# Kernel optimization log

Hardware: AMD Instinct MI355X
Metric: run time of the kernel (lower is better)

The kernel has to match this reference:

```python
import jax, jax.numpy as jnp
import numpy as np

B, N, D, H = 4, 4096, 128, 8
DH = D // H
EPS = 1e-6


def _layernorm(x, g, b):
    mu = jnp.mean(x, axis=-1, keepdims=True)
    var = jnp.var(x, axis=-1, keepdims=True)
    return (x - mu) * jax.lax.rsqrt(var + EPS) * g + b


def setup_inputs() -> dict:
    key = jax.random.key(0)
    ks = jax.random.split(key, 12)
    p = lambda k, shape: (jax.random.normal(k, shape, jnp.float32) * 0.02)
    x = jax.random.normal(ks[0], (B, N, D), jnp.float32)
    # scale fx so the sigmoid of the N-length contraction is not fully saturated
    fx = jax.random.normal(ks[1], (B, N, D), jnp.float32) / N
    return {
        "x": x,
        "fx": fx,
        "ln1_g": jnp.ones((D,), jnp.float32),
        "ln1_b": jnp.zeros((D,), jnp.float32),
        "wq": p(ks[2], (D, D)),
        "wk": p(ks[3], (D, D)),
        "wv": p(ks[4], (D, D)),
        "wo": p(ks[5], (D, D)),
        "bo": jnp.zeros((D,), jnp.float32),
        "ln2_g": jnp.ones((D,), jnp.float32),
        "ln2_b": jnp.zeros((D,), jnp.float32),
        "w1": p(ks[6], (D, D)),
        "b1": jnp.zeros((D,), jnp.float32),
        "w2": p(ks[7], (D, D)),
        "b2": jnp.zeros((D,), jnp.float32),
    }


def reference(x, fx, ln1_g, ln1_b, wq, wk, wv, wo, bo, ln2_g, ln2_b, w1, b1, w2, b2):
    b, n, d = x.shape
    h, dh = H, d // H
    # --- pre-norm linear self-attention ---
    xn = _layernorm(x, ln1_g, ln1_b)
    def heads(w):  # [b,n,d] @ w^T -> [b,h,n,dh]
        return jnp.einsum('bnd,ed->bne', xn, w).reshape(b, n, h, dh).transpose(0, 2, 1, 3)
    q = jax.nn.softmax(heads(wq), axis=-1)   # softmax over feature dim
    k = jax.nn.softmax(heads(wk), axis=2)    # softmax over sequence dim
    v = heads(wv)
    ctx = jnp.einsum('bhnd,bhne->bhde', k, v)         # [b,h,dh,dh]
    attn = jnp.einsum('bhnd,bhde->bhne', q, ctx)       # [b,h,n,dh]
    attn = attn.transpose(0, 2, 1, 3).reshape(b, n, d)
    attn = jnp.einsum('bnd,ed->bne', attn, wo) + bo
    x = x + attn                                       # residual (dropout=identity)
    # --- pre-norm MLP ---
    y = _layernorm(x, ln2_g, ln2_b)
    y = jax.nn.gelu(jnp.einsum('bnd,ed->bne', y, w1) + b1, approximate=False)
    y = jnp.einsum('bnd,ed->bne', y, w2) + b2
    x = x + y
    # --- quadratic update: sigmoid((x x^T) fx), as written in the module ---
    gram = jnp.einsum('bnd,bmd->bnm', x, x)            # [b,n,n] materialized, faithful
    fx = jax.nn.sigmoid(jnp.einsum('bnm,bmd->bnd', gram, fx))
    return (x, fx)
```

## Files before the change

### kernel.cpp

```cpp
#include <hip/hip_runtime.h>
#include <math.h>

#define BB 4
#define NN 4096
#define DD 128
#define MM (BB*NN)

typedef __attribute__((ext_vector_type(8))) short short8;
typedef __attribute__((ext_vector_type(4))) float f32x4;

__device__ inline short f2bf(float f) {
    unsigned u = __float_as_uint(f);
    u = (u + 0x7FFFu + ((u >> 16) & 1u)) >> 16;
    return (short)u;
}
__device__ inline float bf2f(short s) {
    return __uint_as_float(((unsigned)(unsigned short)s) << 16);
}
__device__ inline short8 pack_bf8(float4 a, float4 b) {
    short8 o;
    o[0] = f2bf(a.x); o[1] = f2bf(a.y); o[2] = f2bf(a.z); o[3] = f2bf(a.w);
    o[4] = f2bf(b.x); o[5] = f2bf(b.y); o[6] = f2bf(b.z); o[7] = f2bf(b.w);
    return o;
}
__device__ inline int swzoff(int row, int col) {
    return ((row * 128 + col) * 2) ^ ((row & 7) << 4);
}

__global__ __launch_bounds__(256) void wprep(const float* __restrict__ w0, const float* __restrict__ w1,
                                             const float* __restrict__ w2, const float* __restrict__ w3,
                                             const float* __restrict__ w4, short* __restrict__ wf) {
    int m = blockIdx.x >> 3;
    int j = (blockIdx.x & 7) * 256 + threadIdx.x;
    const float* W = (m == 0) ? w0 : (m == 1) ? w1 : (m == 2) ? w2 : (m == 3) ? w3 : w4;
    int nt = j >> 8, ks = (j >> 6) & 3, l = j & 63, r = l & 15, g = l >> 4;
    const float* src = W + (size_t)(nt * 16 + r) * DD + 32 * ks + 8 * g;
    float4 a = *(const float4*)src;
    float4 b = *(const float4*)(src + 4);
    ((short8*)(wf + (size_t)m * 16384))[j] = pack_bf8(a, b);
}

__global__ __launch_bounds__(256) void lnqkv(const float* __restrict__ x,
                                             const float* __restrict__ lng,
                                             const float* __restrict__ lnb,
                                             const short* __restrict__ wf,
                                             short* __restrict__ qb,
                                             short* __restrict__ ekb,
                                             short* __restrict__ vb) {
    int t = threadIdx.x;
    int block_row = blockIdx.x * 32;
    int w = t >> 6, l = t & 63, r = l & 15, g = l >> 4;
    int row0 = block_row + ((w >> 1) << 4);
    int nt0 = (w & 1) << 2;

    const float* ap = x + (size_t)(row0 + r) * DD + 8 * g;
    float4 av0[4], av1[4];
    #pragma unroll
    for (int ks = 0; ks < 4; ks++) {
        av0[ks] = *(const float4*)(ap + 32 * ks);
        av1[ks] = *(const float4*)(ap + 32 * ks + 4);
    }
    float s = 0.f, ss = 0.f;
    #pragma unroll
    for (int ks = 0; ks < 4; ks++) {
        float4 a = av0[ks], b = av1[ks];
        s  += a.x + a.y + a.z + a.w + b.x + b.y + b.z + b.w;
        ss += a.x*a.x + a.y*a.y + a.z*a.z + a.w*a.w + b.x*b.x + b.y*b.y + b.z*b.z + b.w*b.w;
    }
    s  += __shfl_xor(s, 16);  s  += __shfl_xor(s, 32);
    ss += __shfl_xor(ss, 16); ss += __shfl_xor(ss, 32);
    float mu = s * (1.0f / DD);
    float var = ss * (1.0f / DD) - mu * mu;
    float rs = rsqrtf(var + 1e-6f);

    short8 af[4];
    #pragma unroll
    for (int ks = 0; ks < 4; ks++) {
        float4 g0 = *(const float4*)(lng + 32 * ks + 8 * g);
        float4 g1 = *(const float4*)(lng + 32 * ks + 8 * g + 4);
        float4 b0 = *(const float4*)(lnb + 32 * ks + 8 * g);
        float4 b1 = *(const float4*)(lnb + 32 * ks + 8 * g + 4);
        float4 n0, n1;
        n0.x = (av0[ks].x - mu) * rs * g0.x + b0.x;
        n0.y = (av0[ks].y - mu) * rs * g0.y + b0.y;
        n0.z = (av0[ks].z - mu) * rs * g0.z + b0.z;
        n0.w = (av0[ks].w - mu) * rs * g0.w + b0.w;
        n1.x = (av1[ks].x - mu) * rs * g1.x + b1.x;
        n1.y = (av1[ks].y - mu) * rs * g1.y + b1.y;
        n1.z = (av1[ks].z - mu) * rs * g1.z + b1.z;
        n1.w = (av1[ks].w - mu) * rs * g1.w + b1.w;
        af[ks] = pack_bf8(n0, n1);
    }

    f32x4 acc[3][4];
    #pragma unroll
    for (int m = 0; m < 3; m++)
        #pragma unroll
        for (int n = 0; n < 4; n++) acc[m][n] = (f32x4){0.f, 0.f, 0.f, 0.f};
    const short8* wp8 = (const short8*)wf;
    #pragma unroll
    for (int ks = 0; ks < 4; ks++)
        #pragma unroll
        for (int m = 0; m < 3; m++)
            #pragma unroll
            for (int n = 0; n < 4; n++)
                acc[m][n] = __builtin_amdgcn_mfma_f32_16x16x32_bf16(
                    af[ks], wp8[(size_t)m * 2048 + ((nt0 + n) * 4 + ks) * 64 + l], acc[m][n], 0, 0, 0);

    #pragma unroll
    for (int n = 0; n < 4; n++) {
        int col = (nt0 + n) * 16 + r;
        #pragma unroll
        for (int j = 0; j < 4; j++) {
            size_t row = (size_t)(row0 + 4 * g + j);
            float e = __expf(acc[0][n][j]);
            float sm = e;
            sm += __shfl_xor(sm, 1); sm += __shfl_xor(sm, 2);
            sm += __shfl_xor(sm, 4); sm += __shfl_xor(sm, 8);
            qb[row * DD + col]  = f2bf(e / sm);
            ekb[row * DD + col] = f2bf(__expf(acc[1][n][j]));
            vb[row * DD + col]  = f2bf(acc[2][n][j]);
        }
    }
}

__global__ __launch_bounds__(256) void fused_mid(const short* __restrict__ qb,
                                                 const short* __restrict__ mtf,
                                                 const float* __restrict__ bo,
                                                 const float* __restrict__ x,
                                                 const float* __restrict__ ln2g,
                                                 const float* __restrict__ ln2b,
                                                 const short* __restrict__ w1f,
                                                 const float* __restrict__ b1,
                                                 const short* __restrict__ w2f,
                                                 const float* __restrict__ b2,
                                                 float* __restrict__ xfinal,
                                                 short* __restrict__ xbf) {
    __shared__ __align__(16) char ex[32 * 128 * 2];
    __shared__ float redS[4][16], redSS[4][16];
    int t = threadIdx.x;
    int block_row = blockIdx.x * 32;
    int w = t >> 6, l = t & 63, r = l & 15, g = l >> 4;
    int rh = w >> 1, nt0 = (w & 1) << 2;
    int row0 = block_row + rh * 16;

    const short8* ap = (const short8*)(qb + (size_t)(row0 + r) * DD + 8 * g);
    short8 af[4];
    #pragma unroll
    for (int ks = 0; ks < 4; ks++) af[ks] = ap[ks * 4];
    const short8* mp = (const short8*)(mtf + (size_t)(block_row >> 12) * 16384);
    f32x4 acc[4];
    #pragma unroll
    for (int n = 0; n < 4; n++) acc[n] = (f32x4){0.f, 0.f, 0.f, 0.f};
    #pragma unroll
    for (int ks = 0; ks < 4; ks++)
        #pragma unroll
        for (int n = 0; n < 4; n++)
            acc[n] = __builtin_amdgcn_mfma_f32_16x16x32_bf16(
                af[ks], mp[((nt0 + n) * 4 + ks) * 64 + l], acc[n], 0, 0, 0);

    float vv[4][4];
    #pragma unroll
    for (int n = 0; n < 4; n++) {
        int col = (nt0 + n) * 16 + r;
        float bv = bo[col];
        #pragma unroll
        for (int j = 0; j < 4; j++)
            vv[n][j] = acc[n][j] + bv + x[(size_t)(row0 + 4 * g + j) * DD + col];
    }

    #pragma unroll
    for (int j = 0; j < 4; j++) {
        float s  = vv[0][j] + vv[1][j] + vv[2][j] + vv[3][j];
        float s2 = vv[0][j]*vv[0][j] + vv[1][j]*vv[1][j] + vv[2][j]*vv[2][j] + vv[3][j]*vv[3][j];
        s  += __shfl_xor(s, 1);  s  += __shfl_xor(s, 2);  s  += __shfl_xor(s, 4);  s  += __shfl_xor(s, 8);
        s2 += __shfl_xor(s2, 1); s2 += __shfl_xor(s2, 2); s2 += __shfl_xor(s2, 4); s2 += __shfl_xor(s2, 8);
        if (r == 0) { redS[w][4 * g + j] = s; redSS[w][4 * g + j] = s2; }
    }
    __syncthreads();
    int base = w & 2;
    #pragma unroll
    for (int j = 0; j < 4; j++) {
        int rr = 4 * g + j;
        float S  = redS[base][rr]  + redS[base + 1][rr];
        float SS = redSS[base][rr] + redSS[base + 1][rr];
        float mu = S * (1.0f / DD);
        float var = SS * (1.0f / DD) - mu * mu;
        float rs = rsqrtf(var + 1e-6f);
        int rowL = rh * 16 + rr;
        #pragma unroll
        for (int n = 0; n < 4; n++) {
            int col = (nt0 + n) * 16 + r;
            float y = (vv[n][j] - mu) * rs * ln2g[col] + ln2b[col];
            *(short*)(ex + swzoff(rowL, col)) = f2bf(y);
        }
    }
    __syncthreads();
    int rrow = rh * 16 + r;
    short8 yf[4];
    #pragma unroll
    for (int ks = 0; ks < 4; ks++)
        yf[ks] = *(const short8*)(ex + swzoff(rrow, 32 * ks + 8 * g));
    __syncthreads();
    const short8* w1p = (const short8*)w1f;
    f32x4 acc2[4];
    #pragma unroll
    for (int n = 0; n < 4; n++) acc2[n] = (f32x4){0.f, 0.f, 0.f, 0.f};
    #pragma unroll
    for (int ks = 0; ks < 4; ks++)
        #pragma unroll
        for (int n = 0; n < 4; n++)
            acc2[n] = __builtin_amdgcn_mfma_f32_16x16x32_bf16(
                yf[ks], w1p[((nt0 + n) * 4 + ks) * 64 + l], acc2[n], 0, 0, 0);
    #pragma unroll
    for (int n = 0; n < 4; n++) {
        int col = (nt0 + n) * 16 + r;
        float bv = b1[col];
        #pragma unroll
        for (int j = 0; j < 4; j++) {
            float v = acc2[n][j] + bv;
            v = 0.5f * v * (1.0f + erff(v * 0.70710678118654752f));
            *(short*)(ex + swzoff(rh * 16 + 4 * g + j, col)) = f2bf(v);
        }
    }
    __syncthreads();
    short8 hf[4];
    #pragma unroll
    for (int ks = 0; ks < 4; ks++)
        hf[ks] = *(const short8*)(ex + swzoff(rrow, 32 * ks + 8 * g));
    const short8* w2p = (const short8*)w2f;
    f32x4 acc3[4];
    #pragma unroll
    for (int n = 0; n < 4; n++) acc3[n] = (f32x4){0.f, 0.f, 0.f, 0.f};
    #pragma unroll
    for (int ks = 0; ks < 4; ks++)
        #pragma unroll
        for (int n = 0; n < 4; n++)
            acc3[n] = __builtin_amdgcn_mfma_f32_16x16x32_bf16(
                hf[ks], w2p[((nt0 + n) * 4 + ks) * 64 + l], acc3[n], 0, 0, 0);
    #pragma unroll
    for (int n = 0; n < 4; n++) {
        int col = (nt0 + n) * 16 + r;
        float bv = b2[col];
        #pragma unroll
        for (int j = 0; j < 4; j++) {
            float v = acc3[n][j] + bv + vv[n][j];
            size_t row = (size_t)(row0 + 4 * g + j);
            xfinal[row * DD + col] = v;
            xbf[row * DD + col] = f2bf(v);
        }
    }
}

__global__ __launch_bounds__(256) void ctxp(const short* __restrict__ ek, const short* __restrict__ v,
                                            float* __restrict__ part, float* __restrict__ pcs) {
    int bi = blockIdx.x;
    int chunk = bi & 7, bh = bi >> 3, h = bh & 7, b = bh >> 3;
    int t = threadIdx.x;
    __shared__ float eks[16 * 132], vs[16 * 132];
    const short* eb = ek + (size_t)b * NN * DD + h * 16;
    const short* vb = v  + (size_t)b * NN * DD + h * 16;
    int d = t >> 4, e = t & 15;
    float acc = 0.f, cs = 0.f;
    for (int sc = 0; sc < 4; sc++) {
        int nb = chunk * 512 + sc * 128;
        __syncthreads();
        {
            int row = t >> 1, half = t & 1;
            short8 es = *(const short8*)(eb + (size_t)(nb + row) * DD + half * 8);
            short8 vsv = *(const short8*)(vb + (size_t)(nb + row) * DD + half * 8);
            #pragma unroll
            for (int i = 0; i < 8; i++) {
                int c = half * 8 + i;
                eks[c * 132 + row] = bf2f(es[i]);
                vs [c * 132 + row] = bf2f(vsv[i]);
            }
        }
        __syncthreads();
        #pragma unroll 8
        for (int r4 = 0; r4 < 128; r4 += 4) {
            float4 ev = *(const float4*)(eks + d * 132 + r4);
            float4 vv = *(const float4*)(vs  + e * 132 + r4);
            acc += ev.x * vv.x + ev.y * vv.y + ev.z * vv.z + ev.w * vv.w;
            cs  += ev.x + ev.y + ev.z + ev.w;
        }
    }
    part[(size_t)bi * 256 + t] = acc;
    if (e == 0) pcs[(size_t)bi * 16 + d] = cs;
}

__global__ __launch_bounds__(256) void build_mt_k(const float* __restrict__ part,
                                                  const float* __restrict__ pcs,
                                                  const float* __restrict__ wo,
                                                  short* __restrict__ mtfrag) {
    int b = blockIdx.x >> 3, nt = blockIdx.x & 7;
    int t = threadIdx.x;
    __shared__ float ctxL[2048];
    __shared__ float csL[128];
    __shared__ float woL[2048];
    #pragma unroll
    for (int i = 0; i < 8; i++) {
        int idx = i * 256 + t;
        int h = idx >> 8, rem = idx & 255;
        const float* pp = part + ((size_t)(b * 8 + h) * 8) * 256 + rem;
        float s = 0.f;
        #pragma unroll
        for (int c = 0; c < 8; c++) s += pp[(size_t)c * 256];
        ctxL[idx] = s;
    }
    if (t < 128) {
        int h = t >> 4, d = t & 15;
        const float* qq = pcs + ((size_t)(b * 8 + h) * 8) * 16 + d;
        float s = 0.f;
        #pragma unroll
        for (int c = 0; c < 8; c++) s += qq[(size_t)c * 16];
        csL[t] = s;
    }
    #pragma unroll
    for (int i = 0; i < 8; i++) {
        int idx = i * 256 + t;
        woL[idx] = wo[(size_t)(nt * 16) * DD + idx];
    }
    __syncthreads();
    int ks = (t >> 6) & 3, l = t & 63, r = l & 15, g = l >> 4;
    short8 o;
    #pragma unroll
    for (int i2 = 0; i2 < 8; i2++) {
        int k = 32 * ks + 8 * g + i2;
        float inv = 1.0f / csL[k];
        const float* wrow = woL + r * DD + (k >> 4) * 16;
        float s = 0.f;
        #pragma unroll
        for (int eo = 0; eo < 16; eo++) s += ctxL[k * 16 + eo] * wrow[eo];
        o[i2] = f2bf(s * inv);
    }
    ((short8*)(mtfrag + (size_t)b * 16384))[nt * 256 + t] = o;
}

__global__ __launch_bounds__(256) void sbuild_p(const short* __restrict__ xf,
                                                const float* __restrict__ fx,
                                                short* __restrict__ part) {
    int b = blockIdx.x >> 6, chunk = blockIdx.x & 63;
    int t = threadIdx.x;
    __shared__ float xs[64 * 128], fs[64 * 128];
    const short* xb = xf + ((size_t)b * NN + chunk * 64) * DD;
    const float* fb = fx + ((size_t)b * NN + chunk * 64) * DD;
    float4* xs4 = (float4*)xs; float4* fs4 = (float4*)fs;
    const short8* xg = (const short8*)xb; const float4* fg = (const float4*)fb;
    #pragma unroll
    for (int i = 0; i < 4; i++) {
        int j = i * 256 + t;
        short8 s8 = xg[j];
        float4 a = {bf2f(s8[0]), bf2f(s8[1]), bf2f(s8[2]), bf2f(s8[3])};
        float4 c = {bf2f(s8[4]), bf2f(s8[5]), bf2f(s8[6]), bf2f(s8[7])};
        xs4[2 * j] = a; xs4[2 * j + 1] = c;
    }
    #pragma unroll
    for (int i = 0; i < 8; i++) {
        int j = i * 256 + t;
        fs4[j] = fg[j];
    }
    __syncthreads();
    int td = t >> 4, te = t & 15;
    float acc[8][8];
    #pragma unroll
    for (int a = 0; a < 8; a++)
        #pragma unroll
        for (int c = 0; c < 8; c++) acc[a][c] = 0.f;
    for (int r = 0; r < 64; r++) {
        float4 x0 = xs4[r * 32 + td * 2], x1 = xs4[r * 32 + td * 2 + 1];
        float4 f0 = fs4[r * 32 + te * 2], f1 = fs4[r * 32 + te * 2 + 1];
        float xv[8] = {x0.x, x0.y, x0.z, x0.w, x1.x, x1.y, x1.z, x1.w};
        float fv[8] = {f0.x, f0.y, f0.z, f0.w, f1.x, f1.y, f1.z, f1.w};
        #pragma unroll
        for (int a = 0; a < 8; a++)
            #pragma unroll
            for (int c = 0; c < 8; c++) acc[a][c] = fmaf(xv[a], fv[c], acc[a][c]);
    }
    short* pb = part + (size_t)blockIdx.x * 16384;
    int d0 = td * 8, e0 = te * 8;
    #pragma unroll
    for (int ei = 0; ei < 8; ei++) {
        short8 o;
        #pragma unroll
        for (int i = 0; i < 8; i++) o[i] = f2bf(acc[i][ei]);
        *(short8*)(pb + (size_t)(e0 + ei) * DD + d0) = o;
    }
}

__global__ __launch_bounds__(256) void sreduce(const short* __restrict__ part,
                                               short* __restrict__ stfrag) {
    int b = blockIdx.x >> 3;
    int j = (blockIdx.x & 7) * 256 + threadIdx.x;
    int nt = j >> 8, ks = (j >> 6) & 3, l = j & 63, r = l & 15, g = l >> 4;
    int c = nt * 16 + r, k0 = 32 * ks + 8 * g;
    const short* pb = part + (size_t)b * 64 * 16384 + (size_t)c * DD + k0;
    float s[8] = {0.f, 0.f, 0.f, 0.f, 0.f, 0.f, 0.f, 0.f};
    for (int ch = 0; ch < 64; ch++) {
        short8 u = *(const short8*)(pb + (size_t)ch * 16384);
        #pragma unroll
        for (int i = 0; i < 8; i++) s[i] += bf2f(u[i]);
    }
    short8 o;
    #pragma unroll
    for (int i = 0; i < 8; i++) o[i] = f2bf(s[i]);
    ((short8*)(stfrag + (size_t)b * 16384))[j] = o;
}

__global__ __launch_bounds__(256) void gemm_sig(const short* __restrict__ A,
                                                const short* __restrict__ wfrag,
                                                float* __restrict__ Cf) {
    int t = threadIdx.x;
    int block_row = blockIdx.x * 32;
    int w = t >> 6, l = t & 63, r = l & 15, g = l >> 4;
    int row0 = block_row + ((w >> 1) << 4);
    int nt0 = (w & 1) << 2;
    const short8* ap = (const short8*)(A + (size_t)(row0 + r) * DD + 8 * g);
    short8 af[4];
    #pragma unroll
    for (int ks = 0; ks < 4; ks++) af[ks] = ap[ks * 4];
    const short8* wp8 = (const short8*)(wfrag + (size_t)(block_row >> 12) * 16384);
    f32x4 acc[4];
    #pragma unroll
    for (int n = 0; n < 4; n++) acc[n] = (f32x4){0.f, 0.f, 0.f, 0.f};
    #pragma unroll
    for (int ks = 0; ks < 4; ks++)
        #pragma unroll
        for (int n = 0; n < 4; n++)
            acc[n] = __builtin_amdgcn_mfma_f32_16x16x32_bf16(
                af[ks], wp8[((nt0 + n) * 4 + ks) * 64 + l], acc[n], 0, 0, 0);
    #pragma unroll
    for (int n = 0; n < 4; n++) {
        int col = (nt0 + n) * 16 + r;
        #pragma unroll
        for (int j = 0; j < 4; j++) {
            float v = 1.0f / (1.0f + __expf(-acc[n][j]));
            Cf[(size_t)(row0 + 4 * g + j) * DD + col] = v;
        }
    }
}

extern "C" void kernel_launch(void* const* d_in, const int* in_sizes, int n_in,
                              void* d_out, int out_size, void* d_ws, size_t ws_size,
                              hipStream_t stream) {
    const float* x    = (const float*)d_in[0];
    const float* fx   = (const float*)d_in[1];
    const float* ln1g = (const float*)d_in[2];
    const float* ln1b = (const float*)d_in[3];
    const float* wq   = (const float*)d_in[4];
    const float* wk   = (const float*)d_in[5];
    const float* wv   = (const float*)d_in[6];
    const float* wo   = (const float*)d_in[7];
    const float* bo   = (const float*)d_in[8];
    const float* ln2g = (const float*)d_in[9];
    const float* ln2b = (const float*)d_in[10];
    const float* w1   = (const float*)d_in[11];
    const float* b1   = (const float*)d_in[12];
    const float* w2   = (const float*)d_in[13];
    const float* b2   = (const float*)d_in[14];

    float* out = (float*)d_out;
    float* xfinal = out;
    float* fxout  = out + (size_t)MM * DD;

    float* ws = (float*)d_ws;
    short* qb   = (short*)ws;
    short* ekb  = (short*)(ws + 1048576);
    short* vb   = (short*)(ws + 2097152);
    short* xbf  = (short*)(ws + 3145728);
    short* partSb = (short*)(ws + 4194304);
    float* tail = ws + 6291456;
    short* wfW  = (short*)tail;
    float* partC = tail + 40960;
    float* pcs   = partC + 65536;
    short* mtf   = (short*)(pcs + 4096);
    short* stf   = mtf + 65536;

    wprep<<<40, 256, 0, stream>>>(wq, wk, wv, w1, w2, wfW);
    lnqkv<<<512, 256, 0, stream>>>(x, ln1g, ln1b, wfW, qb, ekb, vb);
    ctxp<<<256, 256, 0, stream>>>(ekb, vb, partC, pcs);
    build_mt_k<<<32, 256, 0, stream>>>(partC, pcs, wo, mtf);
    fused_mid<<<512, 256, 0, stream>>>(qb, mtf, bo, x, ln2g, ln2b,
                                       wfW + 3 * 16384, b1, wfW + 4 * 16384, b2,
                                       xfinal, xbf);
    sbuild_p<<<256, 256, 0, stream>>>(xbf, fx, partSb);
    sreduce<<<32, 256, 0, stream>>>(partSb, stf);
    gemm_sig<<<512, 256, 0, stream>>>(xbf, stf, fxout);
}
```

Baseline: 78.07 us.

## Fuse context reduction into LN/QKV kernel and recompute Q in mid kernel

The LN1+projection kernel now computes only K and V, keeps exp(K) and V in shared memory, and reduces each 32-row tile's per-head K^T V context and column sums directly into global accumulators with atomics. This removes the bf16 q/ek/v intermediate buffers and the separate ctxp kernel. The mid kernel recomputes LN1 and the Q projection with softmax itself, and reuses the loaded x for the residual. sreduce is also split across 8 lanes per output with shuffle reduction for more parallelism. The cost is atomic contention, a memset, and duplicated LN1 work.

Measured after the change: 111.4 us. 42.7% more time.

```diff
diff --git a/kernel.cpp b/kernel.cpp
--- a/kernel.cpp
+++ b/kernel.cpp
@@ -40,18 +40,19 @@
     ((short8*)(wf + (size_t)m * 16384))[j] = pack_bf8(a, b);
 }
 
-__global__ __launch_bounds__(256) void lnqkv(const float* __restrict__ x,
+__global__ __launch_bounds__(256) void lnctx(const float* __restrict__ x,
                                              const float* __restrict__ lng,
                                              const float* __restrict__ lnb,
                                              const short* __restrict__ wf,
-                                             short* __restrict__ qb,
-                                             short* __restrict__ ekb,
-                                             short* __restrict__ vb) {
+                                             float* __restrict__ ctxacc,
+                                             float* __restrict__ csacc) {
+    __shared__ float ekL[32][132];
+    __shared__ float vL[32][132];
     int t = threadIdx.x;
     int block_row = blockIdx.x * 32;
     int w = t >> 6, l = t & 63, r = l & 15, g = l >> 4;
-    int row0 = block_row + ((w >> 1) << 4);
-    int nt0 = (w & 1) << 2;
+    int rh = w >> 1, nt0 = (w & 1) << 2;
+    int row0 = block_row + rh * 16;
 
     const float* ap = x + (size_t)(row0 + r) * DD + 8 * g;
     float4 av0[4], av1[4];
@@ -92,16 +93,16 @@
         af[ks] = pack_bf8(n0, n1);
     }
 
-    f32x4 acc[3][4];
-    #pragma unroll
-    for (int m = 0; m < 3; m++)
+    f32x4 acc[2][4];
+    #pragma unroll
+    for (int m = 0; m < 2; m++)
         #pragma unroll
         for (int n = 0; n < 4; n++) acc[m][n] = (f32x4){0.f, 0.f, 0.f, 0.f};
     const short8* wp8 = (const short8*)wf;
     #pragma unroll
     for (int ks = 0; ks < 4; ks++)
         #pragma unroll
-        for (int m = 0; m < 3; m++)
+        for (int m = 0; m < 2; m++)
             #pragma unroll
             for (int n = 0; n < 4; n++)
                 acc[m][n] = __builtin_amdgcn_mfma_f32_16x16x32_bf16(
@@ -112,22 +113,70 @@
         int col = (nt0 + n) * 16 + r;
         #pragma unroll
         for (int j = 0; j < 4; j++) {
-            size_t row = (size_t)(row0 + 4 * g + j);
-            float e = __expf(acc[0][n][j]);
-            float sm = e;
-            sm += __shfl_xor(sm, 1); sm += __shfl_xor(sm, 2);
-            sm += __shfl_xor(sm, 4); sm += __shfl_xor(sm, 8);
-            qb[row * DD + col]  = f2bf(e / sm);
-            ekb[row * DD + col] = f2bf(__expf(acc[1][n][j]));
-            vb[row * DD + col]  = f2bf(acc[2][n][j]);
-        }
-    }
-}
-
-__global__ __launch_bounds__(256) void fused_mid(const short* __restrict__ qb,
+            int rowL = rh * 16 + 4 * g + j;
+            ekL[rowL][col] = __expf(acc[0][n][j]);
+            vL[rowL][col]  = acc[1][n][j];
+        }
+    }
+    __syncthreads();
+
+    int h = t >> 5, sub = t & 31, d = sub >> 1, e0 = (sub & 1) * 8;
+    int b = block_row >> 12;
+    float cs = 0.f;
+    float sc[8] = {0.f, 0.f, 0.f, 0.f, 0.f, 0.f, 0.f, 0.f};
+    #pragma unroll 8
+    for (int row = 0; row < 32; row++) {
+        float ekv = ekL[row][h * 16 + d];
+        float4 v0 = *(const float4*)&vL[row][h * 16 + e0];
+        float4 v1 = *(const float4*)&vL[row][h * 16 + e0 + 4];
+        sc[0] += ekv * v0.x; sc[1] += ekv * v0.y; sc[2] += ekv * v0.z; sc[3] += ekv * v0.w;
+        sc[4] += ekv * v1.x; sc[5] += ekv * v1.y; sc[6] += ekv * v1.z; sc[7] += ekv * v1.w;
+        cs += ekv;
+    }
+    float* cb = ctxacc + b * 2048 + h * 256 + d * 16 + e0;
+    #pragma unroll
+    for (int i = 0; i < 8; i++) atomicAdd(cb + i, sc[i]);
+    if ((sub & 1) == 0) atomicAdd(csacc + b * 128 + h * 16 + d, cs);
+}
+
+__global__ __launch_bounds__(256) void build_mt_k(const float* __restrict__ ctxacc,
+                                                  const float* __restrict__ csacc,
+                                                  const float* __restrict__ wo,
+                                                  short* __restrict__ mtfrag) {
+    int b = blockIdx.x >> 3, nt = blockIdx.x & 7;
+    int t = threadIdx.x;
+    __shared__ float ctxL[2048];
+    __shared__ float csL[128];
+    __shared__ float woL[2048];
+    #pragma unroll
+    for (int i = 0; i < 8; i++) {
+        int idx = i * 256 + t;
+        ctxL[idx] = ctxacc[(size_t)b * 2048 + idx];
+        woL[idx]  = wo[(size_t)(nt * 16) * DD + idx];
+    }
+    if (t < 128) csL[t] = csacc[b * 128 + t];
+    __syncthreads();
+    int ks = (t >> 6) & 3, l = t & 63, r = l & 15, g = l >> 4;
+    short8 o;
+    #pragma unroll
+    for (int i2 = 0; i2 < 8; i2++) {
+        int k = 32 * ks + 8 * g + i2;
+        float inv = 1.0f / csL[k];
+        const float* wrow = woL + r * DD + (k >> 4) * 16;
+        float s = 0.f;
+        #pragma unroll
+        for (int eo = 0; eo < 16; eo++) s += ctxL[k * 16 + eo] * wrow[eo];
+        o[i2] = f2bf(s * inv);
+    }
+    ((short8*)(mtfrag + (size_t)b * 16384))[nt * 256 + t] = o;
+}
+
+__global__ __launch_bounds__(256) void fused_mid(const float* __restrict__ x,
+                                                 const float* __restrict__ ln1g,
+                                                 const float* __restrict__ ln1b,
+                                                 const short* __restrict__ wqf,
                                                  const short* __restrict__ mtf,
                                                  const float* __restrict__ bo,
-                                                 const float* __restrict__ x,
                                                  const float* __restrict__ ln2g,
                                                  const float* __restrict__ ln2b,
                                                  const short* __restrict__ w1f,
@@ -137,17 +186,95 @@
                                                  float* __restrict__ xfinal,
                                                  short* __restrict__ xbf) {
     __shared__ __align__(16) char ex[32 * 128 * 2];
+    __shared__ float ex2f[32][132];
     __shared__ float redS[4][16], redSS[4][16];
     int t = threadIdx.x;
     int block_row = blockIdx.x * 32;
     int w = t >> 6, l = t & 63, r = l & 15, g = l >> 4;
     int rh = w >> 1, nt0 = (w & 1) << 2;
     int row0 = block_row + rh * 16;
-
-    const short8* ap = (const short8*)(qb + (size_t)(row0 + r) * DD + 8 * g);
+    int rrow = rh * 16 + r;
+
+    const float* ap = x + (size_t)(row0 + r) * DD + 8 * g;
+    float4 av0[4], av1[4];
+    #pragma unroll
+    for (int ks = 0; ks < 4; ks++) {
+        av0[ks] = *(const float4*)(ap + 32 * ks);
+        av1[ks] = *(const float4*)(ap + 32 * ks + 4);
+    }
+    if ((w & 1) == 0) {
+        #pragma unroll
+        for (int ks = 0; ks < 4; ks++) {
+            *(float4*)&ex2f[rrow][32 * ks + 8 * g]     = av0[ks];
+            *(float4*)&ex2f[rrow][32 * ks + 8 * g + 4] = av1[ks];
+        }
+    }
+    float s = 0.f, ss = 0.f;
+    #pragma unroll
+    for (int ks = 0; ks < 4; ks++) {
+        float4 a = av0[ks], b = av1[ks];
+        s  += a.x + a.y + a.z + a.w + b.x + b.y + b.z + b.w;
+        ss += a.x*a.x + a.y*a.y + a.z*a.z + a.w*a.w + b.x*b.x + b.y*b.y + b.z*b.z + b.w*b.w;
+    }
+    s  += __shfl_xor(s, 16);  s  += __shfl_xor(s, 32);
+    ss += __shfl_xor(ss, 16); ss += __shfl_xor(ss, 32);
+    float mu1 = s * (1.0f / DD);
+    float var1 = ss * (1.0f / DD) - mu1 * mu1;
+    float rs1 = rsqrtf(var1 + 1e-6f);
     short8 af[4];
     #pragma unroll
-    for (int ks = 0; ks < 4; ks++) af[ks] = ap[ks * 4];
+    for (int ks = 0; ks < 4; ks++) {
+        float4 g0 = *(const float4*)(ln1g + 32 * ks + 8 * g);
+        float4 g1 = *(const float4*)(ln1g + 32 * ks + 8 * g + 4);
+        float4 b0 = *(const float4*)(ln1b + 32 * ks + 8 * g);
+        float4 b1v = *(const float4*)(ln1b + 32 * ks + 8 * g + 4);
+        float4 n0, n1;
+        n0.x = (av0[ks].x - mu1) * rs1 * g0.x + b0.x;
+        n0.y = (av0[ks].y - mu1) * rs1 * g0.y + b0.y;
+        n0.z = (av0[ks].z - mu1) * rs1 * g0.z + b0.z;
+        n0.w = (av0[ks].w - mu1) * rs1 * g0.w + b0.w;
+        n1.x = (av1[ks].x - mu1) * rs1 * g1.x + b1v.x;
+        n1.y = (av1[ks].y - mu1) * rs1 * g1.y + b1v.y;
+        n1.z = (av1[ks].z - mu1) * rs1 * g1.z + b1v.z;
+        n1.w = (av1[ks].w - mu1) * rs1 * g1.w + b1v.w;
+        af[ks] = pack_bf8(n0, n1);
+    }
+
+    const short8* qp = (const short8*)wqf;
+    f32x4 accq[4];
+    #pragma unroll
+    for (int n = 0; n < 4; n++) accq[n] = (f32x4){0.f, 0.f, 0.f, 0.f};
+    #pragma unroll
+    for (int ks = 0; ks < 4; ks++)
+        #pragma unroll
+        for (int n = 0; n < 4; n++)
+            accq[n] = __builtin_amdgcn_mfma_f32_16x16x32_bf16(
+                af[ks], qp[((nt0 + n) * 4 + ks) * 64 + l], accq[n], 0, 0, 0);
+    #pragma unroll
+    for (int n = 0; n < 4; n++) {
+        int col = (nt0 + n) * 16 + r;
+        #pragma unroll
+        for (int j = 0; j < 4; j++) {
+            float e = __expf(accq[n][j]);
+            float sm = e;
+            sm += __shfl_xor(sm, 1); sm += __shfl_xor(sm, 2);
+            sm += __shfl_xor(sm, 4); sm += __shfl_xor(sm, 8);
+            *(short*)(ex + swzoff(rh * 16 + 4 * g + j, col)) = f2bf(e / sm);
+        }
+    }
+    __syncthreads();
+
+    short8 qf[4];
+    #pragma unroll
+    for (int ks = 0; ks < 4; ks++)
+        qf[ks] = *(const short8*)(ex + swzoff(rrow, 32 * ks + 8 * g));
+    float xres[4][4];
+    #pragma unroll
+    for (int n = 0; n < 4; n++)
+        #pragma unroll
+        for (int j = 0; j < 4; j++)
+            xres[n][j] = ex2f[rh * 16 + 4 * g + j][(nt0 + n) * 16 + r];
+
     const short8* mp = (const short8*)(mtf + (size_t)(block_row >> 12) * 16384);
     f32x4 acc[4];
     #pragma unroll
@@ -157,7 +284,7 @@
         #pragma unroll
         for (int n = 0; n < 4; n++)
             acc[n] = __builtin_amdgcn_mfma_f32_16x16x32_bf16(
-                af[ks], mp[((nt0 + n) * 4 + ks) * 64 + l], acc[n], 0, 0, 0);
+                qf[ks], mp[((nt0 + n) * 4 + ks) * 64 + l], acc[n], 0, 0, 0);
 
     float vv[4][4];
     #pragma unroll
@@ -166,16 +293,16 @@
         float bv = bo[col];
         #pragma unroll
         for (int j = 0; j < 4; j++)
-            vv[n][j] = acc[n][j] + bv + x[(size_t)(row0 + 4 * g + j) * DD + col];
+            vv[n][j] = acc[n][j] + bv + xres[n][j];
     }
 
     #pragma unroll
     for (int j = 0; j < 4; j++) {
-        float s  = vv[0][j] + vv[1][j] + vv[2][j] + vv[3][j];
+        float s1  = vv[0][j] + vv[1][j] + vv[2][j] + vv[3][j];
         float s2 = vv[0][j]*vv[0][j] + vv[1][j]*vv[1][j] + vv[2][j]*vv[2][j] + vv[3][j]*vv[3][j];
-        s  += __shfl_xor(s, 1);  s  += __shfl_xor(s, 2);  s  += __shfl_xor(s, 4);  s  += __shfl_xor(s, 8);
+        s1 += __shfl_xor(s1, 1); s1 += __shfl_xor(s1, 2); s1 += __shfl_xor(s1, 4); s1 += __shfl_xor(s1, 8);
         s2 += __shfl_xor(s2, 1); s2 += __shfl_xor(s2, 2); s2 += __shfl_xor(s2, 4); s2 += __shfl_xor(s2, 8);
-        if (r == 0) { redS[w][4 * g + j] = s; redSS[w][4 * g + j] = s2; }
+        if (r == 0) { redS[w][4 * g + j] = s1; redSS[w][4 * g + j] = s2; }
     }
     __syncthreads();
     int base = w & 2;
@@ -196,7 +323,6 @@
         }
     }
     __syncthreads();
-    int rrow = rh * 16 + r;
     short8 yf[4];
     #pragma unroll
     for (int ks = 0; ks < 4; ks++)
@@ -250,91 +376,6 @@
             xbf[row * DD + col] = f2bf(v);
         }
     }
-}
-
-__global__ __launch_bounds__(256) void ctxp(const short* __restrict__ ek, const short* __restrict__ v,
-                                            float* __restrict__ part, float* __restrict__ pcs) {
-    int bi = blockIdx.x;
-    int chunk = bi & 7, bh = bi >> 3, h = bh & 7, b = bh >> 3;
-    int t = threadIdx.x;
-    __shared__ float eks[16 * 132], vs[16 * 132];
-    const short* eb = ek + (size_t)b * NN * DD + h * 16;
-    const short* vb = v  + (size_t)b * NN * DD + h * 16;
-    int d = t >> 4, e = t & 15;
-    float acc = 0.f, cs = 0.f;
-    for (int sc = 0; sc < 4; sc++) {
-        int nb = chunk * 512 + sc * 128;
-        __syncthreads();
-        {
-            int row = t >> 1, half = t & 1;
-            short8 es = *(const short8*)(eb + (size_t)(nb + row) * DD + half * 8);
-            short8 vsv = *(const short8*)(vb + (size_t)(nb + row) * DD + half * 8);
-            #pragma unroll
-            for (int i = 0; i < 8; i++) {
-                int c = half * 8 + i;
-                eks[c * 132 + row] = bf2f(es[i]);
-                vs [c * 132 + row] = bf2f(vsv[i]);
-            }
-        }
-        __syncthreads();
-        #pragma unroll 8
-        for (int r4 = 0; r4 < 128; r4 += 4) {
-            float4 ev = *(const float4*)(eks + d * 132 + r4);
-            float4 vv = *(const float4*)(vs  + e * 132 + r4);
-            acc += ev.x * vv.x + ev.y * vv.y + ev.z * vv.z + ev.w * vv.w;
-            cs  += ev.x + ev.y + ev.z + ev.w;
-        }
-    }
-    part[(size_t)bi * 256 + t] = acc;
-    if (e == 0) pcs[(size_t)bi * 16 + d] = cs;
-}
-
-__global__ __launch_bounds__(256) void build_mt_k(const float* __restrict__ part,
-                                                  const float* __restrict__ pcs,
-                                                  const float* __restrict__ wo,
-                                                  short* __restrict__ mtfrag) {
-    int b = blockIdx.x >> 3, nt = blockIdx.x & 7;
-    int t = threadIdx.x;
-    __shared__ float ctxL[2048];
-    __shared__ float csL[128];
-    __shared__ float woL[2048];
-    #pragma unroll
-    for (int i = 0; i < 8; i++) {
-        int idx = i * 256 + t;
-        int h = idx >> 8, rem = idx & 255;
-        const float* pp = part + ((size_t)(b * 8 + h) * 8) * 256 + rem;
-        float s = 0.f;
-        #pragma unroll
-        for (int c = 0; c < 8; c++) s += pp[(size_t)c * 256];
-        ctxL[idx] = s;
-    }
-    if (t < 128) {
-        int h = t >> 4, d = t & 15;
-        const float* qq = pcs + ((size_t)(b * 8 + h) * 8) * 16 + d;
-        float s = 0.f;
-        #pragma unroll
-        for (int c = 0; c < 8; c++) s += qq[(size_t)c * 16];
-        csL[t] = s;
-    }
-    #pragma unroll
-    for (int i = 0; i < 8; i++) {
-        int idx = i * 256 + t;
-        woL[idx] = wo[(size_t)(nt * 16) * DD + idx];
-    }
-    __syncthreads();
-    int ks = (t >> 6) & 3, l = t & 63, r = l & 15, g = l >> 4;
-    short8 o;
-    #pragma unroll
-    for (int i2 = 0; i2 < 8; i2++) {
-        int k = 32 * ks + 8 * g + i2;
-        float inv = 1.0f / csL[k];
-        const float* wrow = woL + r * DD + (k >> 4) * 16;
-        float s = 0.f;
-        #pragma unroll
-        for (int eo = 0; eo < 16; eo++) s += ctxL[k * 16 + eo] * wrow[eo];
-        o[i2] = f2bf(s * inv);
-    }
-    ((short8*)(mtfrag + (size_t)b * 16384))[nt * 256 + t] = o;
 }
 
 __global__ __launch_bounds__(256) void sbuild_p(const short* __restrict__ xf,
@@ -390,21 +431,29 @@
 
 __global__ __launch_bounds__(256) void sreduce(const short* __restrict__ part,
                                                short* __restrict__ stfrag) {
-    int b = blockIdx.x >> 3;
-    int j = (blockIdx.x & 7) * 256 + threadIdx.x;
+    int b = blockIdx.x >> 6, grp = blockIdx.x & 63;
+    int t = threadIdx.x;
+    int slotL = t >> 3, sub = t & 7;
+    int j = grp * 32 + slotL;
     int nt = j >> 8, ks = (j >> 6) & 3, l = j & 63, r = l & 15, g = l >> 4;
     int c = nt * 16 + r, k0 = 32 * ks + 8 * g;
     const short* pb = part + (size_t)b * 64 * 16384 + (size_t)c * DD + k0;
     float s[8] = {0.f, 0.f, 0.f, 0.f, 0.f, 0.f, 0.f, 0.f};
-    for (int ch = 0; ch < 64; ch++) {
+    for (int ch = sub; ch < 64; ch += 8) {
         short8 u = *(const short8*)(pb + (size_t)ch * 16384);
         #pragma unroll
         for (int i = 0; i < 8; i++) s[i] += bf2f(u[i]);
     }
-    short8 o;
-    #pragma unroll
-    for (int i = 0; i < 8; i++) o[i] = f2bf(s[i]);
-    ((short8*)(stfrag + (size_t)b * 16384))[j] = o;
+    #pragma unroll
+    for (int o = 1; o <= 4; o <<= 1)
+        #pragma unroll
+        for (int i = 0; i < 8; i++) s[i] += __shfl_xor(s[i], o);
+    if (sub == 0) {
+        short8 o;
+        #pragma unroll
+        for (int i = 0; i < 8; i++) o[i] = f2bf(s[i]);
+        ((short8*)(stfrag + (size_t)b * 16384))[j] = o;
+    }
 }
 
 __global__ __launch_bounds__(256) void gemm_sig(const short* __restrict__ A,
@@ -464,26 +513,22 @@
     float* fxout  = out + (size_t)MM * DD;
 
     float* ws = (float*)d_ws;
-    short* qb   = (short*)ws;
-    short* ekb  = (short*)(ws + 1048576);
-    short* vb   = (short*)(ws + 2097152);
-    short* xbf  = (short*)(ws + 3145728);
-    short* partSb = (short*)(ws + 4194304);
-    float* tail = ws + 6291456;
-    short* wfW  = (short*)tail;
-    float* partC = tail + 40960;
-    float* pcs   = partC + 65536;
-    short* mtf   = (short*)(pcs + 4096);
-    short* stf   = mtf + 65536;
-
+    short* xbf    = (short*)ws;
+    short* partSb = (short*)(ws + 1048576);
+    short* wfW    = (short*)(ws + 3145728);
+    float* ctxacc = ws + 3145728 + 40960;
+    float* csacc  = ctxacc + 8192;
+    short* mtf    = (short*)(csacc + 512);
+    short* stf    = mtf + 65536;
+
+    hipMemsetAsync(ctxacc, 0, (8192 + 512) * sizeof(float), stream);
     wprep<<<40, 256, 0, stream>>>(wq, wk, wv, w1, w2, wfW);
-    lnqkv<<<512, 256, 0, stream>>>(x, ln1g, ln1b, wfW, qb, ekb, vb);
-    ctxp<<<256, 256, 0, stream>>>(ekb, vb, partC, pcs);
-    build_mt_k<<<32, 256, 0, stream>>>(partC, pcs, wo, mtf);
-    fused_mid<<<512, 256, 0, stream>>>(qb, mtf, bo, x, ln2g, ln2b,
+    lnctx<<<512, 256, 0, stream>>>(x, ln1g, ln1b, wfW + 16384, ctxacc, csacc);
+    build_mt_k<<<32, 256, 0, stream>>>(ctxacc, csacc, wo, mtf);
+    fused_mid<<<512, 256, 0, stream>>>(x, ln1g, ln1b, wfW, mtf, bo, ln2g, ln2b,
                                        wfW + 3 * 16384, b1, wfW + 4 * 16384, b2,
                                        xfinal, xbf);
     sbuild_p<<<256, 256, 0, stream>>>(xbf, fx, partSb);
-    sreduce<<<32, 256, 0, stream>>>(partSb, stf);
+    sreduce<<<256, 256, 0, stream>>>(partSb, stf);
     gemm_sig<<<512, 256, 0, stream>>>(xbf, stf, fxout);
 }
```
